# Kernel tuning notes

Measured on AMD Instinct MI355X. Metric: run time of the kernel, lower is better.

## Reference

```python
import jax, jax.numpy as jnp
import numpy as np

B, N, D = 2, 2048, 768
H = 12
HD = D // H
SCALE = HD ** -0.5
EPS = 1e-8


def exp0(v, c):
    # Poincare exponential map at origin: tanh(sqrt(c)||v||) * v / (sqrt(c)||v||)
    sc = jnp.sqrt(c)
    n = jnp.sqrt(jnp.sum(v * v, axis=-1, keepdims=True))
    n = jnp.maximum(n, EPS)
    return jnp.tanh(sc * n) * v / (sc * n)


def log0(x, c):
    # Poincare log map at origin: artanh(sqrt(c)||x||) * x / (sqrt(c)||x||)
    sc = jnp.sqrt(c)
    n = jnp.sqrt(jnp.sum(x * x, axis=-1, keepdims=True))
    n = jnp.maximum(n, EPS)
    t = jnp.clip(sc * n, 0.0, 1.0 - 1e-7)
    return jnp.arctanh(t) * x / (sc * n)


def setup_inputs() -> dict:
    key = jax.random.key(0)
    k1, k2, k3 = jax.random.split(key, 3)
    c0 = 0.1
    x = jax.random.normal(k1, (B, N, D), dtype=jnp.float32)
    # rescale so sqrt(c)*||x|| = 0.5 -> valid points strictly inside the ball
    xn = jnp.sqrt(jnp.sum(x * x, axis=-1, keepdims=True))
    x = x * (0.5 / (np.sqrt(c0) * jnp.maximum(xn, EPS)))
    w_qkv = jax.random.normal(k2, (3 * D, D), dtype=jnp.float32) * (D ** -0.5)
    w_proj = jax.random.normal(k3, (D, D), dtype=jnp.float32) * (D ** -0.5)
    b_proj = jnp.zeros((D,), dtype=jnp.float32)
    curvature = jnp.asarray(c0, dtype=jnp.float32)
    return {"x": x, "w_qkv": w_qkv, "w_proj": w_proj, "b_proj": b_proj,
            "curvature": curvature}


def reference(x, w_qkv, w_proj, b_proj, curvature):
    c = curvature
    v = log0(x, c)                                   # [B,N,D] tangent vectors
    qkv = jnp.einsum('bnd,ed->bne', v, w_qkv)        # [B,N,3D]
    qkv = qkv.reshape(B, N, 3, H, HD).transpose(2, 0, 3, 1, 4)  # [3,B,H,N,HD]
    q, k, v_proj = qkv[0], qkv[1], qkv[2]
    # Map q,k back onto the manifold for the hyperbolic distance score
    qm = exp0(q, c)                                  # [B,H,N,HD]
    km = exp0(k, c)
    q_nsq = jnp.sum(qm * qm, axis=-1)                # [B,H,N]
    k_nsq = jnp.sum(km * km, axis=-1)                # [B,H,N]
    dot = jnp.einsum('bhnd,bhmd->bhnm', qm, km)      # [B,H,N,N]
    # ||q-k||^2 = ||q||^2 + ||k||^2 - 2 q.k  (avoids [B,H,N,N,HD] intermediate)
    diff_sq = jnp.maximum(q_nsq[..., :, None] + k_nsq[..., None, :] - 2.0 * dot, 0.0)
    q_cl = jnp.minimum(q_nsq, 0.99)
    k_cl = jnp.minimum(k_nsq, 0.99)
    denom = (1.0 - q_cl)[..., :, None] * (1.0 - k_cl)[..., None, :] + 1e-8
    inner = jnp.maximum(1.0 + 2.0 * diff_sq / denom, 1.0 + 1e-7)
    distances = jnp.arccosh(inner)                   # [B,H,N,N]
    scores = -distances * SCALE
    attn = jax.nn.softmax(scores, axis=-1)
    out = jnp.einsum('bhnm,bhmd->bhnd', attn, v_proj)
    out = out.transpose(0, 2, 1, 3).reshape(B, N, D)
    v_out = jnp.einsum('bnd,ed->bne', out, w_proj) + b_proj
    return exp0(v_out, c)                            # [B,N,D] on manifold
```

## Files before the change

### kernel.cpp

```cpp
#include <hip/hip_runtime.h>
#include <cmath>

#define ROWS 4096
#define DIM 768
#define QKV_COLS 2304
#define NHEAD 12
#define HEAD_DIM 64
#define SEQ 2048
#define PADK 72

static constexpr float SCALE_F = 0.125f;
static constexpr float EPS_F   = 1e-8f;

typedef __bf16 bfrag __attribute__((ext_vector_type(8)));
typedef float  f32x4 __attribute__((ext_vector_type(4)));

__device__ __forceinline__ float wave_sum64(float v) {
#pragma unroll
  for (int off = 1; off < 64; off <<= 1) v += __shfl_xor(v, off, 64);
  return v;
}

__device__ __forceinline__ unsigned short f2bf(float f) {
  unsigned u = __float_as_uint(f);
  u += 0x7fffu + ((u >> 16) & 1u);
  return (unsigned short)(u >> 16);
}

__device__ __forceinline__ float tanh_over_x(float x) {
  const float e  = __builtin_amdgcn_exp2f(x * 2.8853900817779268f);
  const float th = (e - 1.0f) * __builtin_amdgcn_rcpf(e + 1.0f);
  return (x < 1e-4f) ? 1.0f : th * __builtin_amdgcn_rcpf(x);
}

__device__ __forceinline__ void gl_lds16(const void* g, void* l) {
  __builtin_amdgcn_global_load_lds((const __attribute__((address_space(1))) void*)g,
                                   (__attribute__((address_space(3))) void*)l, 16, 0, 0);
}

__global__ __launch_bounds__(256) void conv_bf16_2(const float* __restrict__ a, int na,
                                                   const float* __restrict__ b, int nb,
                                                   unsigned short* __restrict__ da,
                                                   unsigned short* __restrict__ db) {
  const int i = (blockIdx.x * 256 + threadIdx.x) * 4;
  const float* s;
  unsigned short* d;
  int j;
  if (i < na) { s = a; d = da; j = i; }
  else { j = i - na; if (j >= nb) return; s = b; d = db; }
  const float4 v = *(const float4*)(s + j);
  ushort4 o;
  o.x = f2bf(v.x); o.y = f2bf(v.y); o.z = f2bf(v.z); o.w = f2bf(v.w);
  *(ushort4*)(d + j) = o;
}

__global__ __launch_bounds__(256) void log0_kernel(const float* __restrict__ x,
                                                   const float* __restrict__ cptr,
                                                   unsigned short* __restrict__ vout) {
  const int lane = threadIdx.x & 63;
  const int row  = (blockIdx.x << 2) + (threadIdx.x >> 6);
  const float* xr = x + (size_t)row * DIM;
  unsigned short* vr = vout + (size_t)row * DIM;
  float vals[12];
  float ss = 0.f;
#pragma unroll
  for (int i = 0; i < 12; ++i) {
    float t = xr[lane + (i << 6)];
    vals[i] = t;
    ss += t * t;
  }
  ss = wave_sum64(ss);
  const float sc  = sqrtf(cptr[0]);
  const float n   = fmaxf(sqrtf(ss), EPS_F);
  const float scn = sc * n;
  const float t   = fminf(scn, 1.0f - 1e-7f);
  const float ath = 0.34657359027997264f *
                    __builtin_amdgcn_logf((1.0f + t) * __builtin_amdgcn_rcpf(1.0f - t));
  const float f   = (scn < 1e-4f) ? 1.0f : ath * __builtin_amdgcn_rcpf(scn);
#pragma unroll
  for (int i = 0; i < 12; ++i) vr[lane + (i << 6)] = f2bf(vals[i] * f);
}

__global__ __launch_bounds__(256) void exp0_out_kernel(const float* __restrict__ vin,
                                                       const float* __restrict__ cptr,
                                                       float* __restrict__ outp) {
  const int lane = threadIdx.x & 63;
  const int row  = (blockIdx.x << 2) + (threadIdx.x >> 6);
  const float* vr = vin + (size_t)row * DIM;
  float* orow = outp + (size_t)row * DIM;
  float vals[12];
  float ss = 0.f;
#pragma unroll
  for (int i = 0; i < 12; ++i) {
    float t = vr[lane + (i << 6)];
    vals[i] = t;
    ss += t * t;
  }
  ss = wave_sum64(ss);
  const float sc  = sqrtf(cptr[0]);
  const float n   = fmaxf(sqrtf(ss), EPS_F);
  const float f   = tanh_over_x(sc * n);
#pragma unroll
  for (int i = 0; i < 12; ++i) orow[lane + (i << 6)] = vals[i] * f;
}

template<int BM, int BN>
__global__ __launch_bounds__(256) void gemm_nt_dbuf(const unsigned short* __restrict__ A,
                                                    const unsigned short* __restrict__ B,
                                                    float* __restrict__ C,
                                                    int M, int Ncols, int K,
                                                    const float* __restrict__ bias) {
  constexpr int FI = BM / 32;
  constexpr int FJ = BN / 32;
  constexpr int CH = BM / 64;
  __shared__ unsigned short As[2][BM * 32];
  __shared__ unsigned short Bs[2][BN * 32];
  const int tid = threadIdx.x;
  const int w = tid >> 6, lane = tid & 63;
  const int lq = lane & 15, quad = lane >> 4;
  const int wr = w >> 1, wc = w & 1;
  const int row0 = blockIdx.y * BM;
  const int col0 = blockIdx.x * BN;
  const int srow  = lane >> 2;
  const int skoff = (lane & 3) << 3;

  f32x4 acc[FI][FJ];
#pragma unroll
  for (int i = 0; i < FI; ++i)
#pragma unroll
    for (int j = 0; j < FJ; ++j) acc[i][j] = (f32x4){0.f, 0.f, 0.f, 0.f};

  auto pf = [&](int k0, int buf) {
#pragma unroll
    for (int c = 0; c < CH; ++c) {
      const int r = c * 64 + w * 16;
      gl_lds16(A + (size_t)(row0 + r + srow) * K + k0 + skoff, &As[buf][r * 32]);
      gl_lds16(B + (size_t)(col0 + r + srow) * K + k0 + skoff, &Bs[buf][r * 32]);
    }
  };

  pf(0, 0);
  const int NIT = K / 32;
  for (int it = 0; it < NIT; ++it) {
    const int buf = it & 1;
    __syncthreads();
    if (it + 1 < NIT) pf((it + 1) * 32, buf ^ 1);

    bfrag af[FI], bfg[FJ];
#pragma unroll
    for (int i = 0; i < FI; ++i)
      af[i] = *(const bfrag*)&As[buf][(wr * (BM / 2) + i * 16 + lq) * 32 + (quad << 3)];
#pragma unroll
    for (int j = 0; j < FJ; ++j)
      bfg[j] = *(const bfrag*)&Bs[buf][(wc * (BN / 2) + j * 16 + lq) * 32 + (quad << 3)];
#pragma unroll
    for (int i = 0; i < FI; ++i)
#pragma unroll
      for (int j = 0; j < FJ; ++j)
        acc[i][j] = __builtin_amdgcn_mfma_f32_16x16x32_bf16(af[i], bfg[j], acc[i][j], 0, 0, 0);
  }

#pragma unroll
  for (int i = 0; i < FI; ++i) {
    const int crow = row0 + wr * (BM / 2) + i * 16 + (quad << 2);
#pragma unroll
    for (int j = 0; j < FJ; ++j) {
      const int col = col0 + wc * (BN / 2) + j * 16 + lq;
      const float bj = bias ? bias[col] : 0.0f;
      float* cp = C + (size_t)crow * Ncols + col;
#pragma unroll
      for (int r = 0; r < 4; ++r)
        cp[(size_t)r * Ncols] = acc[i][j][r] + bj;
    }
  }
}

__global__ __launch_bounds__(256) void qkv_prep(const float* __restrict__ qkv,
                                                const float* __restrict__ cptr,
                                                unsigned short* __restrict__ qh,
                                                unsigned short* __restrict__ kh,
                                                unsigned short* __restrict__ vth,
                                                float2* __restrict__ qn2,
                                                float2* __restrict__ kn2) {
  const int qt = blockIdx.x, h = blockIdx.y, b = blockIdx.z;
  const int bh = b * NHEAD + h;
  const int tid = threadIdx.x;
  const int w = tid >> 6, lane = tid & 63;
  const float sc = sqrtf(cptr[0]);

#pragma unroll 2
  for (int t = 0; t < 32; ++t) {
    const int vv = w * 32 + t;
    const int which = vv & 1;
    const int r = vv >> 1;
    const int n = qt * 64 + r;
    const float v = qkv[((size_t)(b * SEQ + n)) * QKV_COLS + which * DIM + h * HEAD_DIM + lane];
    const float ss = wave_sum64(v * v);
    const float nn = fmaxf(sqrtf(ss), EPS_F);
    const float f  = tanh_over_x(sc * nn);
    (which ? kh : qh)[((size_t)bh * SEQ + n) * HEAD_DIM + lane] = f2bf(v * f);
    if (lane == 0) {
      const float nrm = ss * f * f;
      (which ? kn2 : qn2)[(size_t)bh * SEQ + n] =
          make_float2(nrm, 1.0f / (1.0f - fminf(nrm, 0.99f)));
    }
  }

  __shared__ unsigned short T[64 * PADK];
  const int r2 = tid >> 2;
  const int c0 = (tid & 3) << 4;
  const float* src = qkv + ((size_t)(b * SEQ + qt * 64 + r2)) * QKV_COLS + 2 * DIM + h * HEAD_DIM + c0;
#pragma unroll
  for (int z = 0; z < 16; z += 4) {
    const float4 v = *(const float4*)(src + z);
    T[(c0 + z + 0) * PADK + r2] = f2bf(v.x);
    T[(c0 + z + 1) * PADK + r2] = f2bf(v.y);
    T[(c0 + z + 2) * PADK + r2] = f2bf(v.z);
    T[(c0 + z + 3) * PADK + r2] = f2bf(v.w);
  }
  __syncthreads();
  const int d  = tid >> 2;
  const int k0 = (tid & 3) << 4;
  unsigned short* dst = vth + ((size_t)bh * HEAD_DIM + d) * SEQ + (size_t)qt * 64 + k0;
  *(uint4*)dst       = *(const uint4*)&T[d * PADK + k0];
  *(uint4*)(dst + 8) = *(const uint4*)&T[d * PADK + k0 + 8];
}

__global__ __launch_bounds__(256) void flash_mfma(const unsigned short* __restrict__ qh,
                                                  const unsigned short* __restrict__ kh,
                                                  const unsigned short* __restrict__ vth,
                                                  const float2* __restrict__ qn2,
                                                  const float2* __restrict__ kn2,
                                                  unsigned short* __restrict__ attn_out) {
  const int flat = blockIdx.x;
  const int bhid = flat % 24;
  const int qt   = flat / 24;
  const int h = bhid % NHEAD, b = bhid / NHEAD;
  const int bh = b * NHEAD + h;
  const int tid = threadIdx.x;
  const int w = tid >> 6, lane = tid & 63;
  const int lq = lane & 15, quad = lane >> 4;

  __shared__ unsigned short Ks[2][64 * 64];
  __shared__ unsigned short Vt[2][64 * 64];
  __shared__ unsigned short Ps[64 * PADK];
  __shared__ float knA[2][64], knB[2][64];

  const unsigned short* qbase = qh + ((size_t)bh * SEQ + (size_t)qt * 64) * HEAD_DIM;
  const float2* qnb = qn2 + (size_t)bh * SEQ + (size_t)qt * 64;
  const float2* knb = kn2 + (size_t)bh * SEQ;

  const int srow = tid >> 3, spos = tid & 7;
  const int sB = spos ^ (srow & 7);
  const char* kgsrc = (const char*)(kh + (size_t)bh * SEQ * HEAD_DIM) + (size_t)srow * 128 + sB * 16;
  const char* vgsrc = (const char*)(vth + (size_t)bh * HEAD_DIM * SEQ) + (size_t)srow * 4096 + sB * 16;

  auto prefetch = [&](int kt, int buf) {
    const char* kp = kgsrc + (size_t)kt * 8192;
    const char* vp = vgsrc + (size_t)kt * 128;
    gl_lds16(kp,          (char*)Ks[buf] + w * 1024);
    gl_lds16(kp + 4096,   (char*)Ks[buf] + 4096 + w * 1024);
    gl_lds16(vp,          (char*)Vt[buf] + w * 1024);
    gl_lds16(vp + 131072, (char*)Vt[buf] + 4096 + w * 1024);
    if (tid < 64) {
      const float2 kv = knb[kt * 64 + tid];
      knA[buf][tid] = kv.x;
      knB[buf][tid] = kv.y;
    }
  };

  bfrag aq[2];
#pragma unroll
  for (int khf = 0; khf < 2; ++khf)
    aq[khf] = *(const bfrag*)(qbase + (size_t)(w * 16 + lq) * HEAD_DIM + khf * 32 + quad * 8);

  const float2 qq = qnb[w * 16 + lq];
  const float qnS = qq.x;
  const float rqS = 2.0f * qq.y;

  bfrag ones;
#pragma unroll
  for (int j = 0; j < 8; ++j) ones[j] = (__bf16)1.0f;

  f32x4 oacc[4];
  f32x4 lacc = (f32x4){0.f, 0.f, 0.f, 0.f};
#pragma unroll
  for (int d = 0; d < 4; ++d) oacc[d] = (f32x4){0.f, 0.f, 0.f, 0.f};
  const int swz = lq & 7;

  prefetch(0, 0);
  for (int kt = 0; kt < SEQ / 64; ++kt) {
    const int buf = kt & 1;
    __syncthreads();
    if (kt + 1 < SEQ / 64) prefetch(kt + 1, buf ^ 1);

    f32x4 s[4];
#pragma unroll
    for (int st = 0; st < 4; ++st) s[st] = (f32x4){0.f, 0.f, 0.f, 0.f};
#pragma unroll
    for (int khf = 0; khf < 2; ++khf)
#pragma unroll
      for (int st = 0; st < 4; ++st) {
        const bfrag ak = *(const bfrag*)&Ks[buf][(st * 16 + lq) * 64 + (((khf << 2) + quad) ^ swz) * 8];
        s[st] = __builtin_amdgcn_mfma_f32_16x16x32_bf16(ak, aq[khf], s[st], 0, 0, 0);
      }

#pragma unroll
    for (int st = 0; st < 4; ++st) {
      const f32x4 kna = *(const f32x4*)&knA[buf][st * 16 + quad * 4];
      const f32x4 knr = *(const f32x4*)&knB[buf][st * 16 + quad * 4];
      unsigned u[4];
#pragma unroll
      for (int i = 0; i < 4; ++i) {
        float tt = fmaf(-2.0f, s[st][i], qnS + kna[i]);
        tt = fmaxf(tt, 0.0f);
        const float inner = fmaf(tt, rqS * knr[i], 1.0f);
        const float root = __builtin_amdgcn_sqrtf(fmaf(inner, inner, -1.0f));
        const float wgt = __builtin_amdgcn_exp2f(-0.125f * __builtin_amdgcn_logf(inner + root));
        u[i] = __float_as_uint(wgt);
      }
      uint2 pk;
      pk.x = __builtin_amdgcn_perm(u[1], u[0], 0x07060302u);
      pk.y = __builtin_amdgcn_perm(u[3], u[2], 0x07060302u);
      *(uint2*)&Ps[(w * 16 + lq) * PADK + st * 16 + quad * 4] = pk;
    }

#pragma unroll
    for (int khf = 0; khf < 2; ++khf) {
      const bfrag ap = *(const bfrag*)&Ps[(w * 16 + lq) * PADK + khf * 32 + quad * 8];
      lacc = __builtin_amdgcn_mfma_f32_16x16x32_bf16(ap, ones, lacc, 0, 0, 0);
#pragma unroll
      for (int d = 0; d < 4; ++d) {
        const bfrag bv = *(const bfrag*)&Vt[buf][(d * 16 + lq) * 64 + (((khf << 2) + quad) ^ swz) * 8];
        oacc[d] = __builtin_amdgcn_mfma_f32_16x16x32_bf16(ap, bv, oacc[d], 0, 0, 0);
      }
    }
  }

  float rl4[4];
#pragma unroll
  for (int i = 0; i < 4; ++i) rl4[i] = __builtin_amdgcn_rcpf(lacc[i]);

  unsigned short* ob = attn_out + ((size_t)b * SEQ + (size_t)qt * 64 + w * 16) * DIM + h * HEAD_DIM;
#pragma unroll
  for (int d = 0; d < 4; ++d)
#pragma unroll
    for (int i = 0; i < 4; ++i)
      ob[(size_t)(quad * 4 + i) * DIM + d * 16 + lq] = f2bf(oacc[d][i] * rl4[i]);
}

extern "C" void kernel_launch(void* const* d_in, const int* in_sizes, int n_in,
                              void* d_out, int out_size, void* d_ws, size_t ws_size,
                              hipStream_t stream) {
  const float* x      = (const float*)d_in[0];
  const float* w_qkv  = (const float*)d_in[1];
  const float* w_proj = (const float*)d_in[2];
  const float* b_proj = (const float*)d_in[3];
  const float* curv   = (const float*)d_in[4];
  float* outp = (float*)d_out;

  float* ws = (float*)d_ws;
  unsigned short* v_tan_bf = (unsigned short*)ws;
  unsigned short* attn_bf  = (unsigned short*)ws;
  float* qkv   = ws + 1572864;
  float* v_out = qkv;
  unsigned short* qh  = (unsigned short*)(qkv + 9437184);
  unsigned short* kh  = qh + 3145728;
  unsigned short* vth = kh + 3145728;
  unsigned short* wqkv_bf  = vth + 3145728;
  unsigned short* wproj_bf = wqkv_bf + 1769472;
  float2* qn2 = (float2*)(wproj_bf + 589824);
  float2* kn2 = qn2 + 49152;

  conv_bf16_2<<<dim3((2359296 / 4 + 255) / 256), dim3(256), 0, stream>>>(
      w_qkv, 1769472, w_proj, 589824, wqkv_bf, wproj_bf);
  log0_kernel<<<dim3(ROWS / 4), dim3(256), 0, stream>>>(x, curv, v_tan_bf);
  gemm_nt_dbuf<128, 128><<<dim3(QKV_COLS / 128, ROWS / 128), dim3(256), 0, stream>>>(
      v_tan_bf, wqkv_bf, qkv, ROWS, QKV_COLS, DIM, nullptr);
  qkv_prep<<<dim3(SEQ / 64, NHEAD, 2), dim3(256), 0, stream>>>(qkv, curv, qh, kh, vth,
                                                               qn2, kn2);
  flash_mfma<<<dim3(768), dim3(256), 0, stream>>>(qh, kh, vth, qn2, kn2, attn_bf);
  gemm_nt_dbuf<64, 64><<<dim3(DIM / 64, ROWS / 64), dim3(256), 0, stream>>>(
      attn_bf, wproj_bf, v_out, ROWS, DIM, DIM, b_proj);
  exp0_out_kernel<<<dim3(ROWS / 4), dim3(256), 0, stream>>>(v_out, curv, outp);
}
```

Baseline: 222.8 us.

## Fuse QKV GEMM epilogue with exp0 prep and merge weight conversion into log0

The QKV GEMM epilogue now applies exp0 to the Q and K tiles, computes their norms, writes bf16 head-major Q/K and transposed V directly, and drops both the fp32 qkv intermediate and the separate qkv_prep kernel. The weight bf16 conversion is merged into the log0 launch, saving one kernel launch. Flash attention now reads the key norm arrays directly from global memory (split into separate A/B arrays) instead of staging them through LDS. The cost is scattered 2-byte stores for the transposed V in the epilogue and per-iteration global loads of the key norms inside flash attention.

New measurement: 205.7 us. -7.7%, faster.

```diff
diff --git a/kernel.cpp b/kernel.cpp
--- a/kernel.cpp
+++ b/kernel.cpp
@@ -9,8 +9,7 @@
 #define SEQ 2048
 #define PADK 72
 
-static constexpr float SCALE_F = 0.125f;
-static constexpr float EPS_F   = 1e-8f;
+static constexpr float EPS_F = 1e-8f;
 
 typedef __bf16 bfrag __attribute__((ext_vector_type(8)));
 typedef float  f32x4 __attribute__((ext_vector_type(4)));
@@ -38,25 +37,26 @@
                                    (__attribute__((address_space(3))) void*)l, 16, 0, 0);
 }
 
-__global__ __launch_bounds__(256) void conv_bf16_2(const float* __restrict__ a, int na,
-                                                   const float* __restrict__ b, int nb,
-                                                   unsigned short* __restrict__ da,
-                                                   unsigned short* __restrict__ db) {
-  const int i = (blockIdx.x * 256 + threadIdx.x) * 4;
-  const float* s;
-  unsigned short* d;
-  int j;
-  if (i < na) { s = a; d = da; j = i; }
-  else { j = i - na; if (j >= nb) return; s = b; d = db; }
-  const float4 v = *(const float4*)(s + j);
-  ushort4 o;
-  o.x = f2bf(v.x); o.y = f2bf(v.y); o.z = f2bf(v.z); o.w = f2bf(v.w);
-  *(ushort4*)(d + j) = o;
-}
-
-__global__ __launch_bounds__(256) void log0_kernel(const float* __restrict__ x,
-                                                   const float* __restrict__ cptr,
-                                                   unsigned short* __restrict__ vout) {
+__global__ __launch_bounds__(256) void log0_conv(const float* __restrict__ x,
+                                                 const float* __restrict__ cptr,
+                                                 unsigned short* __restrict__ vout,
+                                                 const float* __restrict__ wa, int na,
+                                                 const float* __restrict__ wb, int nb,
+                                                 unsigned short* __restrict__ da,
+                                                 unsigned short* __restrict__ db) {
+  if (blockIdx.x >= ROWS / 4) {
+    const int i = ((blockIdx.x - ROWS / 4) * 256 + threadIdx.x) * 4;
+    const float* s;
+    unsigned short* d;
+    int j;
+    if (i < na) { s = wa; d = da; j = i; }
+    else { j = i - na; if (j >= nb) return; s = wb; d = db; }
+    const float4 v = *(const float4*)(s + j);
+    ushort4 o;
+    o.x = f2bf(v.x); o.y = f2bf(v.y); o.z = f2bf(v.z); o.w = f2bf(v.w);
+    *(ushort4*)(d + j) = o;
+    return;
+  }
   const int lane = threadIdx.x & 63;
   const int row  = (blockIdx.x << 2) + (threadIdx.x >> 6);
   const float* xr = x + (size_t)row * DIM;
@@ -97,9 +97,9 @@
     ss += t * t;
   }
   ss = wave_sum64(ss);
-  const float sc  = sqrtf(cptr[0]);
-  const float n   = fmaxf(sqrtf(ss), EPS_F);
-  const float f   = tanh_over_x(sc * n);
+  const float sc = sqrtf(cptr[0]);
+  const float n  = fmaxf(sqrtf(ss), EPS_F);
+  const float f  = tanh_over_x(sc * n);
 #pragma unroll
   for (int i = 0; i < 12; ++i) orow[lane + (i << 6)] = vals[i] * f;
 }
@@ -175,62 +175,121 @@
   }
 }
 
-__global__ __launch_bounds__(256) void qkv_prep(const float* __restrict__ qkv,
-                                                const float* __restrict__ cptr,
-                                                unsigned short* __restrict__ qh,
-                                                unsigned short* __restrict__ kh,
-                                                unsigned short* __restrict__ vth,
-                                                float2* __restrict__ qn2,
-                                                float2* __restrict__ kn2) {
-  const int qt = blockIdx.x, h = blockIdx.y, b = blockIdx.z;
-  const int bh = b * NHEAD + h;
+__global__ __launch_bounds__(256) void gemm_qkv_fused(const unsigned short* __restrict__ A,
+                                                      const unsigned short* __restrict__ B,
+                                                      const float* __restrict__ cptr,
+                                                      unsigned short* __restrict__ qh,
+                                                      unsigned short* __restrict__ kh,
+                                                      unsigned short* __restrict__ vth,
+                                                      float* __restrict__ qnA,
+                                                      float* __restrict__ qnB,
+                                                      float* __restrict__ knA,
+                                                      float* __restrict__ knB) {
+  __shared__ unsigned short As[2][128 * 32];
+  __shared__ unsigned short Bs[2][128 * 32];
   const int tid = threadIdx.x;
   const int w = tid >> 6, lane = tid & 63;
-  const float sc = sqrtf(cptr[0]);
-
-#pragma unroll 2
-  for (int t = 0; t < 32; ++t) {
-    const int vv = w * 32 + t;
-    const int which = vv & 1;
-    const int r = vv >> 1;
-    const int n = qt * 64 + r;
-    const float v = qkv[((size_t)(b * SEQ + n)) * QKV_COLS + which * DIM + h * HEAD_DIM + lane];
-    const float ss = wave_sum64(v * v);
-    const float nn = fmaxf(sqrtf(ss), EPS_F);
-    const float f  = tanh_over_x(sc * nn);
-    (which ? kh : qh)[((size_t)bh * SEQ + n) * HEAD_DIM + lane] = f2bf(v * f);
-    if (lane == 0) {
-      const float nrm = ss * f * f;
-      (which ? kn2 : qn2)[(size_t)bh * SEQ + n] =
-          make_float2(nrm, 1.0f / (1.0f - fminf(nrm, 0.99f)));
-    }
-  }
-
-  __shared__ unsigned short T[64 * PADK];
-  const int r2 = tid >> 2;
-  const int c0 = (tid & 3) << 4;
-  const float* src = qkv + ((size_t)(b * SEQ + qt * 64 + r2)) * QKV_COLS + 2 * DIM + h * HEAD_DIM + c0;
-#pragma unroll
-  for (int z = 0; z < 16; z += 4) {
-    const float4 v = *(const float4*)(src + z);
-    T[(c0 + z + 0) * PADK + r2] = f2bf(v.x);
-    T[(c0 + z + 1) * PADK + r2] = f2bf(v.y);
-    T[(c0 + z + 2) * PADK + r2] = f2bf(v.z);
-    T[(c0 + z + 3) * PADK + r2] = f2bf(v.w);
-  }
-  __syncthreads();
-  const int d  = tid >> 2;
-  const int k0 = (tid & 3) << 4;
-  unsigned short* dst = vth + ((size_t)bh * HEAD_DIM + d) * SEQ + (size_t)qt * 64 + k0;
-  *(uint4*)dst       = *(const uint4*)&T[d * PADK + k0];
-  *(uint4*)(dst + 8) = *(const uint4*)&T[d * PADK + k0 + 8];
+  const int lq = lane & 15, quad = lane >> 4;
+  const int wr = w >> 1, wc = w & 1;
+  const int row0 = blockIdx.y << 7;
+  const int col0 = blockIdx.x << 7;
+  const int srow  = lane >> 2;
+  const int skoff = (lane & 3) << 3;
+
+  f32x4 acc[4][4];
+#pragma unroll
+  for (int i = 0; i < 4; ++i)
+#pragma unroll
+    for (int j = 0; j < 4; ++j) acc[i][j] = (f32x4){0.f, 0.f, 0.f, 0.f};
+
+  auto pf = [&](int k0, int buf) {
+#pragma unroll
+    for (int c = 0; c < 2; ++c) {
+      const int r = c * 64 + w * 16;
+      gl_lds16(A + (size_t)(row0 + r + srow) * DIM + k0 + skoff, &As[buf][r * 32]);
+      gl_lds16(B + (size_t)(col0 + r + srow) * DIM + k0 + skoff, &Bs[buf][r * 32]);
+    }
+  };
+
+  pf(0, 0);
+  for (int it = 0; it < DIM / 32; ++it) {
+    const int buf = it & 1;
+    __syncthreads();
+    if (it + 1 < DIM / 32) pf((it + 1) * 32, buf ^ 1);
+
+    bfrag af[4], bfg[4];
+#pragma unroll
+    for (int i = 0; i < 4; ++i)
+      af[i] = *(const bfrag*)&As[buf][((wr << 6) + (i << 4) + lq) * 32 + (quad << 3)];
+#pragma unroll
+    for (int j = 0; j < 4; ++j)
+      bfg[j] = *(const bfrag*)&Bs[buf][((wc << 6) + (j << 4) + lq) * 32 + (quad << 3)];
+#pragma unroll
+    for (int i = 0; i < 4; ++i)
+#pragma unroll
+      for (int j = 0; j < 4; ++j)
+        acc[i][j] = __builtin_amdgcn_mfma_f32_16x16x32_bf16(af[i], bfg[j], acc[i][j], 0, 0, 0);
+  }
+
+  const int colw = col0 + (wc << 6);
+  const int seg  = colw / DIM;
+  const int hh   = (colw % DIM) >> 6;
+  const int rowb = row0 + (wr << 6);
+
+  if (seg == 2) {
+#pragma unroll
+    for (int i = 0; i < 4; ++i)
+#pragma unroll
+      for (int r = 0; r < 4; ++r) {
+        const int rowg = rowb + (i << 4) + (quad << 2) + r;
+        const int bh = (rowg >> 11) * NHEAD + hh;
+        const int n_ = rowg & 2047;
+#pragma unroll
+        for (int j = 0; j < 4; ++j)
+          vth[((size_t)bh * HEAD_DIM + (j << 4) + lq) * SEQ + n_] = f2bf(acc[i][j][r]);
+      }
+  } else {
+    unsigned short* dst = seg ? kh : qh;
+    float* nA = seg ? knA : qnA;
+    float* nB = seg ? knB : qnB;
+    const float sc = sqrtf(cptr[0]);
+#pragma unroll
+    for (int i = 0; i < 4; ++i)
+#pragma unroll
+      for (int r = 0; r < 4; ++r) {
+        float ss = acc[i][0][r] * acc[i][0][r];
+        ss = fmaf(acc[i][1][r], acc[i][1][r], ss);
+        ss = fmaf(acc[i][2][r], acc[i][2][r], ss);
+        ss = fmaf(acc[i][3][r], acc[i][3][r], ss);
+        ss += __shfl_xor(ss, 1, 64);
+        ss += __shfl_xor(ss, 2, 64);
+        ss += __shfl_xor(ss, 4, 64);
+        ss += __shfl_xor(ss, 8, 64);
+        const float nn = fmaxf(sqrtf(ss), EPS_F);
+        const float f  = tanh_over_x(sc * nn);
+        const int rowg = rowb + (i << 4) + (quad << 2) + r;
+        const int bh = (rowg >> 11) * NHEAD + hh;
+        const int n_ = rowg & 2047;
+        unsigned short* rp = dst + ((size_t)bh * SEQ + n_) * HEAD_DIM;
+#pragma unroll
+        for (int j = 0; j < 4; ++j)
+          rp[(j << 4) + lq] = f2bf(acc[i][j][r] * f);
+        if (lq == 0) {
+          const float nrm = ss * f * f;
+          nA[(size_t)bh * SEQ + n_] = nrm;
+          nB[(size_t)bh * SEQ + n_] = 1.0f / (1.0f - fminf(nrm, 0.99f));
+        }
+      }
+  }
 }
 
 __global__ __launch_bounds__(256) void flash_mfma(const unsigned short* __restrict__ qh,
                                                   const unsigned short* __restrict__ kh,
                                                   const unsigned short* __restrict__ vth,
-                                                  const float2* __restrict__ qn2,
-                                                  const float2* __restrict__ kn2,
+                                                  const float* __restrict__ qnA,
+                                                  const float* __restrict__ qnB,
+                                                  const float* __restrict__ knA,
+                                                  const float* __restrict__ knB,
                                                   unsigned short* __restrict__ attn_out) {
   const int flat = blockIdx.x;
   const int bhid = flat % 24;
@@ -244,11 +303,10 @@
   __shared__ unsigned short Ks[2][64 * 64];
   __shared__ unsigned short Vt[2][64 * 64];
   __shared__ unsigned short Ps[64 * PADK];
-  __shared__ float knA[2][64], knB[2][64];
 
   const unsigned short* qbase = qh + ((size_t)bh * SEQ + (size_t)qt * 64) * HEAD_DIM;
-  const float2* qnb = qn2 + (size_t)bh * SEQ + (size_t)qt * 64;
-  const float2* knb = kn2 + (size_t)bh * SEQ;
+  const float* knAb = knA + (size_t)bh * SEQ;
+  const float* knBb = knB + (size_t)bh * SEQ;
 
   const int srow = tid >> 3, spos = tid & 7;
   const int sB = spos ^ (srow & 7);
@@ -262,11 +320,6 @@
     gl_lds16(kp + 4096,   (char*)Ks[buf] + 4096 + w * 1024);
     gl_lds16(vp,          (char*)Vt[buf] + w * 1024);
     gl_lds16(vp + 131072, (char*)Vt[buf] + 4096 + w * 1024);
-    if (tid < 64) {
-      const float2 kv = knb[kt * 64 + tid];
-      knA[buf][tid] = kv.x;
-      knB[buf][tid] = kv.y;
-    }
   };
 
   bfrag aq[2];
@@ -274,9 +327,8 @@
   for (int khf = 0; khf < 2; ++khf)
     aq[khf] = *(const bfrag*)(qbase + (size_t)(w * 16 + lq) * HEAD_DIM + khf * 32 + quad * 8);
 
-  const float2 qq = qnb[w * 16 + lq];
-  const float qnS = qq.x;
-  const float rqS = 2.0f * qq.y;
+  const float qnS = qnA[(size_t)bh * SEQ + qt * 64 + w * 16 + lq];
+  const float rqS = 2.0f * qnB[(size_t)bh * SEQ + qt * 64 + w * 16 + lq];
 
   bfrag ones;
 #pragma unroll
@@ -291,8 +343,16 @@
   prefetch(0, 0);
   for (int kt = 0; kt < SEQ / 64; ++kt) {
     const int buf = kt & 1;
+    const int key0 = kt * 64;
     __syncthreads();
     if (kt + 1 < SEQ / 64) prefetch(kt + 1, buf ^ 1);
+
+    f32x4 kna[4], knr[4];
+#pragma unroll
+    for (int st = 0; st < 4; ++st) {
+      kna[st] = *(const f32x4*)(knAb + key0 + st * 16 + (quad << 2));
+      knr[st] = *(const f32x4*)(knBb + key0 + st * 16 + (quad << 2));
+    }
 
     f32x4 s[4];
 #pragma unroll
@@ -307,14 +367,12 @@
 
 #pragma unroll
     for (int st = 0; st < 4; ++st) {
-      const f32x4 kna = *(const f32x4*)&knA[buf][st * 16 + quad * 4];
-      const f32x4 knr = *(const f32x4*)&knB[buf][st * 16 + quad * 4];
       unsigned u[4];
 #pragma unroll
       for (int i = 0; i < 4; ++i) {
-        float tt = fmaf(-2.0f, s[st][i], qnS + kna[i]);
+        float tt = fmaf(-2.0f, s[st][i], qnS + kna[st][i]);
         tt = fmaxf(tt, 0.0f);
-        const float inner = fmaf(tt, rqS * knr[i], 1.0f);
+        const float inner = fmaf(tt, rqS * knr[st][i], 1.0f);
         const float root = __builtin_amdgcn_sqrtf(fmaf(inner, inner, -1.0f));
         const float wgt = __builtin_amdgcn_exp2f(-0.125f * __builtin_amdgcn_logf(inner + root));
         u[i] = __float_as_uint(wgt);
@@ -362,24 +420,22 @@
   float* ws = (float*)d_ws;
   unsigned short* v_tan_bf = (unsigned short*)ws;
   unsigned short* attn_bf  = (unsigned short*)ws;
-  float* qkv   = ws + 1572864;
-  float* v_out = qkv;
-  unsigned short* qh  = (unsigned short*)(qkv + 9437184);
+  float* v_out = ws + 1572864;
+  unsigned short* qh  = (unsigned short*)(v_out + 3145728);
   unsigned short* kh  = qh + 3145728;
   unsigned short* vth = kh + 3145728;
   unsigned short* wqkv_bf  = vth + 3145728;
   unsigned short* wproj_bf = wqkv_bf + 1769472;
-  float2* qn2 = (float2*)(wproj_bf + 589824);
-  float2* kn2 = qn2 + 49152;
-
-  conv_bf16_2<<<dim3((2359296 / 4 + 255) / 256), dim3(256), 0, stream>>>(
-      w_qkv, 1769472, w_proj, 589824, wqkv_bf, wproj_bf);
-  log0_kernel<<<dim3(ROWS / 4), dim3(256), 0, stream>>>(x, curv, v_tan_bf);
-  gemm_nt_dbuf<128, 128><<<dim3(QKV_COLS / 128, ROWS / 128), dim3(256), 0, stream>>>(
-      v_tan_bf, wqkv_bf, qkv, ROWS, QKV_COLS, DIM, nullptr);
-  qkv_prep<<<dim3(SEQ / 64, NHEAD, 2), dim3(256), 0, stream>>>(qkv, curv, qh, kh, vth,
-                                                               qn2, kn2);
-  flash_mfma<<<dim3(768), dim3(256), 0, stream>>>(qh, kh, vth, qn2, kn2, attn_bf);
+  float* qnA = (float*)(wproj_bf + 589824);
+  float* qnB = qnA + 49152;
+  float* knA = qnB + 49152;
+  float* knB = knA + 49152;
+
+  log0_conv<<<dim3(ROWS / 4 + 2304), dim3(256), 0, stream>>>(
+      x, curv, v_tan_bf, w_qkv, 1769472, w_proj, 589824, wqkv_bf, wproj_bf);
+  gemm_qkv_fused<<<dim3(QKV_COLS / 128, ROWS / 128), dim3(256), 0, stream>>>(
+      v_tan_bf, wqkv_bf, curv, qh, kh, vth, qnA, qnB, knA, knB);
+  flash_mfma<<<dim3(768), dim3(256), 0, stream>>>(qh, kh, vth, qnA, qnB, knA, knB, attn_bf);
   gemm_nt_dbuf<64, 64><<<dim3(DIM / 64, ROWS / 64), dim3(256), 0, stream>>>(
       attn_bf, wproj_bf, v_out, ROWS, DIM, DIM, b_proj);
   exp0_out_kernel<<<dim3(ROWS / 4), dim3(256), 0, stream>>>(v_out, curv, outp);
```
